# Performance work log

Hardware: AMD Instinct MI355X
Metric: run time of the kernel (lower is better)

Reference implementation:

```python
import jax, jax.numpy as jnp
import numpy as np

B, H, W, D = 4, 64, 64, 256
NH = 8
HD = D // NH        # 32
R = 2               # reduction_ratio
SCALE = 1.0 / np.sqrt(HD).astype(np.float32)
EPS = 1e-5


def _layernorm(x, g, b):
    m = jnp.mean(x, axis=-1, keepdims=True)
    v = jnp.mean((x - m) ** 2, axis=-1, keepdims=True)
    return (x - m) * jax.lax.rsqrt(v + EPS) * g + b


def setup_inputs() -> dict:
    key = jax.random.key(0)
    ks = jax.random.split(key, 8)
    s = 0.02
    return {
        "x": jax.random.normal(ks[0], (B, H, W, D), jnp.float32),
        "de": jax.random.normal(ks[1], (B, H, W, D), jnp.float32),  # unused by module
        "ln1_g": jnp.ones((D,), jnp.float32),
        "ln1_b": jnp.zeros((D,), jnp.float32),
        "Wq": jax.random.normal(ks[2], (D, D), jnp.float32) * s,
        "bq": jnp.zeros((D,), jnp.float32),
        "Wk": jax.random.normal(ks[3], (D, D), jnp.float32) * s,
        "bk": jnp.zeros((D,), jnp.float32),
        "Wv": jax.random.normal(ks[4], (D, D), jnp.float32) * s,
        "bv": jnp.zeros((D,), jnp.float32),
        "Wmean": jax.random.normal(ks[5], (D, D), jnp.float32) * s,  # no bias
        "ln2_g": jnp.ones((D,), jnp.float32),
        "ln2_b": jnp.zeros((D,), jnp.float32),
        "Wo": jax.random.normal(ks[6], (D, D), jnp.float32) * s,
        "bo": jnp.zeros((D,), jnp.float32),
    }


def reference(x, de, ln1_g, ln1_b, Wq, bq, Wk, bk, Wv, bv, Wmean, ln2_g, ln2_b, Wo, bo):
    b, h, w, d = x.shape
    identity = x
    x_norm = _layernorm(x, ln1_g, ln1_b)
    q = x_norm @ Wq + bq                                   # [b,h,w,d]
    # shift_size == 0 -> no roll. Block-mean pool K/V by factor R.
    x_red = jnp.mean(x.reshape(b, h // R, R, w // R, R, d), axis=(2, 4))  # [b,h/R,w/R,d]
    x_red = x_red @ Wmean
    x_red_norm = _layernorm(x_red, ln2_g, ln2_b)
    k = x_red_norm @ Wk + bk
    v = x_red_norm @ Wv + bv
    # split heads: [b, NH, N, HD]
    qf = q.reshape(b, h * w, NH, HD).transpose(0, 2, 1, 3)
    kf = k.reshape(b, (h // R) * (w // R), NH, HD).transpose(0, 2, 1, 3)
    vf = v.reshape(b, (h // R) * (w // R), NH, HD).transpose(0, 2, 1, 3)
    attn = jax.nn.softmax(jnp.einsum('bhqd,bhkd->bhqk', qf, kf) * SCALE, axis=-1)
    out = jnp.einsum('bhqk,bhkd->bhqd', attn, vf)          # [b,NH,N,HD]
    out = out.transpose(0, 2, 1, 3).reshape(b, h, w, d)
    out = out @ Wo + bo
    out = out + identity
    return out, attn
```

## Files before the change

### kernel.cpp

```cpp
#include <hip/hip_runtime.h>

typedef __bf16 bf16x8 __attribute__((ext_vector_type(8)));
typedef __bf16 bf16x4 __attribute__((ext_vector_type(4)));
typedef float f32x4 __attribute__((ext_vector_type(4)));

#define SCALE 0.17677669529663687f

template<int MODE>
__device__ __forceinline__ void gemm_body(const __bf16* __restrict__ A,
    const __bf16* __restrict__ Wt, const float* __restrict__ bias,
    const float* __restrict__ resid, void* __restrict__ Cout,
    int bx, int by, int tid) {
  const int w = tid >> 6, l = tid & 63;
  const int col = l & 15, quad = l >> 4;
  const int row0 = bx * 64 + w * 16;
  const int col0 = by * 64;
  f32x4 acc[4] = {{0.f,0.f,0.f,0.f},{0.f,0.f,0.f,0.f},{0.f,0.f,0.f,0.f},{0.f,0.f,0.f,0.f}};
  const __bf16* ap = A + (size_t)(row0 + col) * 256 + quad * 8;
  #pragma unroll
  for (int ks = 0; ks < 8; ++ks) {
    bf16x8 af = *(const bf16x8*)(ap + ks * 32);
    #pragma unroll
    for (int n = 0; n < 4; ++n) {
      bf16x8 bf = *(const bf16x8*)(Wt + (size_t)(col0 + n * 16 + col) * 256 + ks * 32 + quad * 8);
      acc[n] = __builtin_amdgcn_mfma_f32_16x16x32_bf16(af, bf, acc[n], 0, 0, 0);
    }
  }
  const int rbase = row0 + quad * 4;
  #pragma unroll
  for (int n = 0; n < 4; ++n) {
    const int cc = col0 + n * 16 + col;
    const float bv = bias ? bias[cc] : 0.0f;
    if (MODE == 0) {
      __bf16* C = (__bf16*)Cout;
      #pragma unroll
      for (int r = 0; r < 4; ++r)
        C[(size_t)(rbase + r) * 256 + cc] = (__bf16)(acc[n][r] + bv);
    } else if (MODE == 1) {
      __bf16* C = (__bf16*)Cout;
      const int bb2 = rbase >> 10, tl = rbase & 1023;
      bf16x4 o4;
      #pragma unroll
      for (int r = 0; r < 4; ++r) o4[r] = (__bf16)(acc[n][r] + bv);
      *(bf16x4*)(C + ((size_t)(bb2 * 256 + cc)) * 1024 + tl) = o4;
    } else {
      float* C = (float*)Cout;
      #pragma unroll
      for (int r = 0; r < 4; ++r) {
        size_t off = (size_t)(rbase + r) * 256 + cc;
        C[off] = acc[n][r] + bv + resid[off];
      }
    }
  }
}

__global__ __launch_bounds__(256) void prep_kernel(
    const float* __restrict__ W0, const float* __restrict__ W1,
    const float* __restrict__ W2, const float* __restrict__ W3,
    const float* __restrict__ W4,
    __bf16* __restrict__ T0, __bf16* __restrict__ T1,
    __bf16* __restrict__ T2, __bf16* __restrict__ T3,
    __bf16* __restrict__ T4,
    const float* __restrict__ x, const float* __restrict__ g1,
    const float* __restrict__ b1, __bf16* __restrict__ xn,
    __bf16* __restrict__ xp) {
  const int blk = blockIdx.x, tid = threadIdx.x;
  if (blk < 1280) {
    int which = blk >> 8;
    const float* W = which == 0 ? W0 : which == 1 ? W1 : which == 2 ? W2 : which == 3 ? W3 : W4;
    __bf16* T = which == 0 ? T0 : which == 1 ? T1 : which == 2 ? T2 : which == 3 ? T3 : T4;
    int id = (blk & 255) * 256 + tid;
    int kk = id >> 8, n = id & 255;
    T[n * 256 + kk] = (__bf16)W[id];
  } else if (blk < 5376) {
    int wid = ((blk - 1280) * 256 + tid) >> 6;
    int lane = tid & 63;
    const float4 v = *(const float4*)(x + (size_t)wid * 256 + lane * 4);
    float s = v.x + v.y + v.z + v.w;
    #pragma unroll
    for (int off = 32; off; off >>= 1) s += __shfl_down(s, off);
    float mean = __shfl(s, 0) * (1.0f / 256.0f);
    float dx = v.x - mean, dy = v.y - mean, dz = v.z - mean, dw = v.w - mean;
    float vs = dx * dx + dy * dy + dz * dz + dw * dw;
    #pragma unroll
    for (int off = 32; off; off >>= 1) vs += __shfl_down(vs, off);
    float rstd = rsqrtf(__shfl(vs, 0) * (1.0f / 256.0f) + 1e-5f);
    const float4 gg = *(const float4*)(g1 + lane * 4);
    const float4 bv = *(const float4*)(b1 + lane * 4);
    bf16x4 o4;
    o4[0] = (__bf16)(dx * rstd * gg.x + bv.x);
    o4[1] = (__bf16)(dy * rstd * gg.y + bv.y);
    o4[2] = (__bf16)(dz * rstd * gg.z + bv.z);
    o4[3] = (__bf16)(dw * rstd * gg.w + bv.w);
    *(bf16x4*)(xn + (size_t)wid * 256 + lane * 4) = o4;
  } else {
    int idx = (blk - 5376) * 256 + tid;
    int t = idx >> 6, c4 = (idx & 63) << 2;
    int b = t >> 10, rem = t & 1023;
    int i = rem >> 5, j = rem & 31;
    size_t base = ((size_t)b * 4096 + i * 128 + j * 2) * 256 + c4;
    float4 a0 = *(const float4*)(x + base);
    float4 a1 = *(const float4*)(x + base + 256);
    float4 a2 = *(const float4*)(x + base + 16384);
    float4 a3 = *(const float4*)(x + base + 16640);
    bf16x4 o4;
    o4[0] = (__bf16)(0.25f * (a0.x + a1.x + a2.x + a3.x));
    o4[1] = (__bf16)(0.25f * (a0.y + a1.y + a2.y + a3.y));
    o4[2] = (__bf16)(0.25f * (a0.z + a1.z + a2.z + a3.z));
    o4[3] = (__bf16)(0.25f * (a0.w + a1.w + a2.w + a3.w));
    *(bf16x4*)(xp + (size_t)t * 256 + c4) = o4;
  }
}

__global__ __launch_bounds__(256) void qm_kernel(
    const __bf16* __restrict__ xn, const __bf16* __restrict__ WtQ,
    const float* __restrict__ bq, __bf16* __restrict__ qb,
    const __bf16* __restrict__ xp, const __bf16* __restrict__ WtM,
    const float* __restrict__ g2, const float* __restrict__ b2,
    __bf16* __restrict__ xr) {
  const int blk = blockIdx.x, tid = threadIdx.x;
  if (blk < 1024) {
    gemm_body<0>(xn, WtQ, bq, nullptr, qb, blk & 255, blk >> 8, tid);
    return;
  }
  const int w = tid >> 6, l = tid & 63;
  const int col = l & 15, quad = l >> 4;
  const int row0 = (blk - 1024) * 64 + w * 16;
  f32x4 acc[16];
  #pragma unroll
  for (int n = 0; n < 16; ++n) acc[n] = (f32x4){0.f, 0.f, 0.f, 0.f};
  const __bf16* ap = xp + (size_t)(row0 + col) * 256 + quad * 8;
  #pragma unroll
  for (int ks = 0; ks < 8; ++ks) {
    bf16x8 af = *(const bf16x8*)(ap + ks * 32);
    #pragma unroll
    for (int n = 0; n < 16; ++n) {
      bf16x8 bf = *(const bf16x8*)(WtM + (size_t)(n * 16 + col) * 256 + ks * 32 + quad * 8);
      acc[n] = __builtin_amdgcn_mfma_f32_16x16x32_bf16(af, bf, acc[n], 0, 0, 0);
    }
  }
  #pragma unroll
  for (int r = 0; r < 4; ++r) {
    float s = 0.f;
    #pragma unroll
    for (int n = 0; n < 16; ++n) s += acc[n][r];
    #pragma unroll
    for (int m = 1; m < 16; m <<= 1) s += __shfl_xor(s, m);
    float mean = s * (1.0f / 256.0f);
    float vs = 0.f;
    #pragma unroll
    for (int n = 0; n < 16; ++n) { float d = acc[n][r] - mean; vs += d * d; }
    #pragma unroll
    for (int m = 1; m < 16; m <<= 1) vs += __shfl_xor(vs, m);
    float rstd = rsqrtf(vs * (1.0f / 256.0f) + 1e-5f);
    int row = row0 + quad * 4 + r;
    #pragma unroll
    for (int n = 0; n < 16; ++n) {
      int cc = n * 16 + col;
      xr[(size_t)row * 256 + cc] = (__bf16)((acc[n][r] - mean) * rstd * g2[cc] + b2[cc]);
    }
  }
}

__global__ __launch_bounds__(256) void kv_kernel(
    const __bf16* __restrict__ xr, const __bf16* __restrict__ WtK,
    const float* __restrict__ bk, __bf16* __restrict__ kbuf,
    const __bf16* __restrict__ WtV, const float* __restrict__ bv,
    __bf16* __restrict__ vTb) {
  const int blk = blockIdx.x, tid = threadIdx.x;
  if (blk < 256) gemm_body<0>(xr, WtK, bk, nullptr, kbuf, blk & 63, blk >> 6, tid);
  else { int k = blk - 256; gemm_body<1>(xr, WtV, bv, nullptr, vTb, k & 63, k >> 6, tid); }
}

__global__ __launch_bounds__(256) void o_kernel(
    const __bf16* __restrict__ oat, const __bf16* __restrict__ WtO,
    const float* __restrict__ bo, const float* __restrict__ resid,
    float* __restrict__ out) {
  gemm_body<2>(oat, WtO, bo, resid, out, blockIdx.x, blockIdx.y, threadIdx.x);
}

__device__ __forceinline__ int swz(int row, int c) {
  return row * 1024 + (c ^ ((row & 7) << 2));
}

__global__ __launch_bounds__(256) void attn_fused(
    const __bf16* __restrict__ q, const __bf16* __restrict__ kb,
    const __bf16* __restrict__ vT, float* __restrict__ attn,
    __bf16* __restrict__ oat) {
  __shared__ float Ss[16 * 1024];
  __shared__ float part[64 * 32];
  __shared__ float inv_s[16];
  const int tid = threadIdx.x;
  const int w = tid >> 6, l = tid & 63;
  const int col = l & 15, quad = l >> 4;
  const int bh = blockIdx.y, b = bh >> 3, h = bh & 7;
  const int q0 = blockIdx.x * 16;

  bf16x8 qf = *(const bf16x8*)(q + ((size_t)(b * 4096 + q0 + col)) * 256 + h * 32 + quad * 8);
  const __bf16* kbase = kb + ((size_t)(b * 1024 + col)) * 256 + h * 32 + quad * 8;
  #pragma unroll 4
  for (int t = 0; t < 16; ++t) {
    int j0 = w * 256 + t * 16;
    bf16x8 kf = *(const bf16x8*)(kbase + (size_t)j0 * 256);
    f32x4 c = {0.f, 0.f, 0.f, 0.f};
    c = __builtin_amdgcn_mfma_f32_16x16x32_bf16(qf, kf, c, 0, 0, 0);
    #pragma unroll
    for (int r = 0; r < 4; ++r)
      Ss[swz(quad * 4 + r, j0 + col)] = c[r] * SCALE;
  }
  __syncthreads();

  #pragma unroll
  for (int rr = 0; rr < 4; ++rr) {
    int row = w * 4 + rr;
    float4 v4[4];
    float m = -1e30f;
    #pragma unroll
    for (int i = 0; i < 4; ++i) {
      v4[i] = *(const float4*)(&Ss[swz(row, i * 256 + l * 4)]);
      m = fmaxf(m, fmaxf(fmaxf(v4[i].x, v4[i].y), fmaxf(v4[i].z, v4[i].w)));
    }
    #pragma unroll
    for (int off = 32; off; off >>= 1) m = fmaxf(m, __shfl_down(m, off));
    m = __shfl(m, 0);
    float s = 0.f;
    #pragma unroll
    for (int i = 0; i < 4; ++i) {
      v4[i].x = __expf(v4[i].x - m); v4[i].y = __expf(v4[i].y - m);
      v4[i].z = __expf(v4[i].z - m); v4[i].w = __expf(v4[i].w - m);
      s += v4[i].x + v4[i].y + v4[i].z + v4[i].w;
    }
    #pragma unroll
    for (int off = 32; off; off >>= 1) s += __shfl_down(s, off);
    if (l == 0) inv_s[row] = 1.0f / __shfl(s, 0);
    #pragma unroll
    for (int i = 0; i < 4; ++i)
      *(float4*)(&Ss[swz(row, i * 256 + l * 4)]) = v4[i];
  }
  __syncthreads();

  {
    float* abase = attn + ((size_t)bh * 4096 + q0) * 1024;
    int c4 = tid * 4;
    #pragma unroll 4
    for (int row = 0; row < 16; ++row) {
      f32x4 pv = *(const f32x4*)(&Ss[swz(row, c4)]);
      float iv = inv_s[row];
      pv[0] *= iv; pv[1] *= iv; pv[2] *= iv; pv[3] *= iv;
      __builtin_nontemporal_store(pv, (f32x4*)(abase + (size_t)row * 1024 + c4));
    }
  }

  f32x4 a0 = {0.f, 0.f, 0.f, 0.f}, a1 = {0.f, 0.f, 0.f, 0.f};
  const __bf16* v0p = vT + ((size_t)(b * 256 + h * 32 + col)) * 1024;
  const __bf16* v1p = v0p + 16 * 1024;
  #pragma unroll 2
  for (int s8 = 0; s8 < 8; ++s8) {
    int k0 = w * 256 + s8 * 32;
    int c0 = k0 + quad * 8;
    f32x4 p0 = *(const f32x4*)(&Ss[swz(col, c0)]);
    f32x4 p1 = *(const f32x4*)(&Ss[swz(col, c0 + 4)]);
    bf16x8 af;
    af[0] = (__bf16)p0[0]; af[1] = (__bf16)p0[1]; af[2] = (__bf16)p0[2]; af[3] = (__bf16)p0[3];
    af[4] = (__bf16)p1[0]; af[5] = (__bf16)p1[1]; af[6] = (__bf16)p1[2]; af[7] = (__bf16)p1[3];
    bf16x8 b0 = *(const bf16x8*)(v0p + k0 + quad * 8);
    bf16x8 b1 = *(const bf16x8*)(v1p + k0 + quad * 8);
    a0 = __builtin_amdgcn_mfma_f32_16x16x32_bf16(af, b0, a0, 0, 0, 0);
    a1 = __builtin_amdgcn_mfma_f32_16x16x32_bf16(af, b1, a1, 0, 0, 0);
  }

  #pragma unroll
  for (int r = 0; r < 4; ++r) {
    part[(w * 16 + quad * 4 + r) * 32 + col] = a0[r];
    part[(w * 16 + quad * 4 + r) * 32 + 16 + col] = a1[r];
  }
  __syncthreads();
  int idx = tid;
  #pragma unroll
  for (int it = 0; it < 2; ++it, idx += 256) {
    int row = idx >> 5, d = idx & 31;
    float sum = (part[row * 32 + d] + part[(16 + row) * 32 + d]
               + part[(32 + row) * 32 + d] + part[(48 + row) * 32 + d]) * inv_s[row];
    oat[((size_t)(b * 4096 + q0 + row)) * 256 + h * 32 + d] = (__bf16)sum;
  }
}

extern "C" void kernel_launch(void* const* d_in, const int* in_sizes, int n_in,
                              void* d_out, int out_size, void* d_ws, size_t ws_size,
                              hipStream_t stream) {
  (void)in_sizes; (void)n_in; (void)out_size; (void)ws_size;
  const float* x     = (const float*)d_in[0];
  const float* ln1_g = (const float*)d_in[2];
  const float* ln1_b = (const float*)d_in[3];
  const float* Wq    = (const float*)d_in[4];
  const float* bq    = (const float*)d_in[5];
  const float* Wk    = (const float*)d_in[6];
  const float* bk    = (const float*)d_in[7];
  const float* Wv    = (const float*)d_in[8];
  const float* bv    = (const float*)d_in[9];
  const float* Wmean = (const float*)d_in[10];
  const float* ln2_g = (const float*)d_in[11];
  const float* ln2_b = (const float*)d_in[12];
  const float* Wo    = (const float*)d_in[13];
  const float* bo    = (const float*)d_in[14];

  float* out  = (float*)d_out;
  float* attn = out + 4194304;

  __bf16* w0   = (__bf16*)d_ws;
  __bf16* xn   = w0;
  __bf16* qb   = w0 + 4194304;
  __bf16* oat  = w0 + 8388608;
  __bf16* xp   = w0 + 12582912;
  __bf16* xr   = w0 + 14680064;
  __bf16* kbuf = w0 + 15728640;
  __bf16* vTb  = w0 + 16777216;
  __bf16* WtQ  = w0 + 17825792;
  __bf16* WtK  = WtQ + 65536;
  __bf16* WtV  = WtK + 65536;
  __bf16* WtM  = WtV + 65536;
  __bf16* WtO  = WtM + 65536;

  prep_kernel<<<6400, 256, 0, stream>>>(Wq, Wk, Wv, Wmean, Wo,
                                        WtQ, WtK, WtV, WtM, WtO,
                                        x, ln1_g, ln1_b, xn, xp);
  qm_kernel<<<1088, 256, 0, stream>>>(xn, WtQ, bq, qb, xp, WtM, ln2_g, ln2_b, xr);
  kv_kernel<<<512, 256, 0, stream>>>(xr, WtK, bk, kbuf, WtV, bv, vTb);
  attn_fused<<<dim3(256, 32), 256, 0, stream>>>(qb, kbuf, vTb, attn, oat);
  o_kernel<<<dim3(256, 4), 256, 0, stream>>>(oat, WtO, bo, x, out);
}
```

Measured before the change: 744.9 us.

## Fuse softmax normalization with attn store, two query tiles per block, coalesce output epilogue

The attention kernel now normalizes probabilities in registers inside the softmax pass and writes them to the global attn tensor straight from there. This removes the separate shared-memory read-back pass and the inv_s array, and the PV result no longer needs rescaling. Each block now handles two 16-row query tiles in sequence, which halves the grid and reuses the per-block K/V pointer setup. The output projection stages its accumulators through shared memory so the residual load and the fp32 output store use coalesced float4 accesses. The trade-offs are less block-level parallelism and extra LDS traffic in the output kernel.

```diff
diff --git a/kernel.cpp b/kernel.cpp
--- a/kernel.cpp
+++ b/kernel.cpp
@@ -9,8 +9,7 @@
 template<int MODE>
 __device__ __forceinline__ void gemm_body(const __bf16* __restrict__ A,
     const __bf16* __restrict__ Wt, const float* __restrict__ bias,
-    const float* __restrict__ resid, void* __restrict__ Cout,
-    int bx, int by, int tid) {
+    void* __restrict__ Cout, int bx, int by, int tid) {
   const int w = tid >> 6, l = tid & 63;
   const int col = l & 15, quad = l >> 4;
   const int row0 = bx * 64 + w * 16;
@@ -36,20 +35,13 @@
       #pragma unroll
       for (int r = 0; r < 4; ++r)
         C[(size_t)(rbase + r) * 256 + cc] = (__bf16)(acc[n][r] + bv);
-    } else if (MODE == 1) {
+    } else {
       __bf16* C = (__bf16*)Cout;
       const int bb2 = rbase >> 10, tl = rbase & 1023;
       bf16x4 o4;
       #pragma unroll
       for (int r = 0; r < 4; ++r) o4[r] = (__bf16)(acc[n][r] + bv);
       *(bf16x4*)(C + ((size_t)(bb2 * 256 + cc)) * 1024 + tl) = o4;
-    } else {
-      float* C = (float*)Cout;
-      #pragma unroll
-      for (int r = 0; r < 4; ++r) {
-        size_t off = (size_t)(rbase + r) * 256 + cc;
-        C[off] = acc[n][r] + bv + resid[off];
-      }
     }
   }
 }
@@ -120,7 +112,7 @@
     __bf16* __restrict__ xr) {
   const int blk = blockIdx.x, tid = threadIdx.x;
   if (blk < 1024) {
-    gemm_body<0>(xn, WtQ, bq, nullptr, qb, blk & 255, blk >> 8, tid);
+    gemm_body<0>(xn, WtQ, bq, qb, blk & 255, blk >> 8, tid);
     return;
   }
   const int w = tid >> 6, l = tid & 63;
@@ -168,15 +160,50 @@
     const __bf16* __restrict__ WtV, const float* __restrict__ bv,
     __bf16* __restrict__ vTb) {
   const int blk = blockIdx.x, tid = threadIdx.x;
-  if (blk < 256) gemm_body<0>(xr, WtK, bk, nullptr, kbuf, blk & 63, blk >> 6, tid);
-  else { int k = blk - 256; gemm_body<1>(xr, WtV, bv, nullptr, vTb, k & 63, k >> 6, tid); }
+  if (blk < 256) gemm_body<0>(xr, WtK, bk, kbuf, blk & 63, blk >> 6, tid);
+  else { int k = blk - 256; gemm_body<1>(xr, WtV, bv, vTb, k & 63, k >> 6, tid); }
 }
 
 __global__ __launch_bounds__(256) void o_kernel(
     const __bf16* __restrict__ oat, const __bf16* __restrict__ WtO,
     const float* __restrict__ bo, const float* __restrict__ resid,
     float* __restrict__ out) {
-  gemm_body<2>(oat, WtO, bo, resid, out, blockIdx.x, blockIdx.y, threadIdx.x);
+  __shared__ float sm[4][16][68];
+  const int tid = threadIdx.x;
+  const int w = tid >> 6, l = tid & 63;
+  const int col = l & 15, quad = l >> 4;
+  const int row0 = blockIdx.x * 64 + w * 16;
+  const int col0 = blockIdx.y * 64;
+  f32x4 acc[4] = {{0.f,0.f,0.f,0.f},{0.f,0.f,0.f,0.f},{0.f,0.f,0.f,0.f},{0.f,0.f,0.f,0.f}};
+  const __bf16* ap = oat + (size_t)(row0 + col) * 256 + quad * 8;
+  #pragma unroll
+  for (int ks = 0; ks < 8; ++ks) {
+    bf16x8 af = *(const bf16x8*)(ap + ks * 32);
+    #pragma unroll
+    for (int n = 0; n < 4; ++n) {
+      bf16x8 bf = *(const bf16x8*)(WtO + (size_t)(col0 + n * 16 + col) * 256 + ks * 32 + quad * 8);
+      acc[n] = __builtin_amdgcn_mfma_f32_16x16x32_bf16(af, bf, acc[n], 0, 0, 0);
+    }
+  }
+  #pragma unroll
+  for (int n = 0; n < 4; ++n) {
+    const float bv = bo[col0 + n * 16 + col];
+    #pragma unroll
+    for (int r = 0; r < 4; ++r)
+      sm[w][quad * 4 + r][n * 16 + col] = acc[n][r] + bv;
+  }
+  #pragma unroll
+  for (int i = 0; i < 4; ++i) {
+    int lr = i * 4 + quad;
+    int f4 = l & 15;
+    size_t off = (size_t)(row0 + lr) * 256 + col0 + f4 * 4;
+    float4 rv = *(const float4*)(resid + off);
+    const float* sp = &sm[w][lr][f4 * 4];
+    float4 ov;
+    ov.x = sp[0] + rv.x; ov.y = sp[1] + rv.y;
+    ov.z = sp[2] + rv.z; ov.w = sp[3] + rv.w;
+    *(float4*)(out + off) = ov;
+  }
 }
 
 __device__ __forceinline__ int swz(int row, int c) {
@@ -189,99 +216,94 @@
     __bf16* __restrict__ oat) {
   __shared__ float Ss[16 * 1024];
   __shared__ float part[64 * 32];
-  __shared__ float inv_s[16];
   const int tid = threadIdx.x;
   const int w = tid >> 6, l = tid & 63;
   const int col = l & 15, quad = l >> 4;
   const int bh = blockIdx.y, b = bh >> 3, h = bh & 7;
-  const int q0 = blockIdx.x * 16;
-
-  bf16x8 qf = *(const bf16x8*)(q + ((size_t)(b * 4096 + q0 + col)) * 256 + h * 32 + quad * 8);
   const __bf16* kbase = kb + ((size_t)(b * 1024 + col)) * 256 + h * 32 + quad * 8;
-  #pragma unroll 4
-  for (int t = 0; t < 16; ++t) {
-    int j0 = w * 256 + t * 16;
-    bf16x8 kf = *(const bf16x8*)(kbase + (size_t)j0 * 256);
-    f32x4 c = {0.f, 0.f, 0.f, 0.f};
-    c = __builtin_amdgcn_mfma_f32_16x16x32_bf16(qf, kf, c, 0, 0, 0);
-    #pragma unroll
-    for (int r = 0; r < 4; ++r)
-      Ss[swz(quad * 4 + r, j0 + col)] = c[r] * SCALE;
-  }
-  __syncthreads();
-
-  #pragma unroll
-  for (int rr = 0; rr < 4; ++rr) {
-    int row = w * 4 + rr;
-    float4 v4[4];
-    float m = -1e30f;
-    #pragma unroll
-    for (int i = 0; i < 4; ++i) {
-      v4[i] = *(const float4*)(&Ss[swz(row, i * 256 + l * 4)]);
-      m = fmaxf(m, fmaxf(fmaxf(v4[i].x, v4[i].y), fmaxf(v4[i].z, v4[i].w)));
-    }
-    #pragma unroll
-    for (int off = 32; off; off >>= 1) m = fmaxf(m, __shfl_down(m, off));
-    m = __shfl(m, 0);
-    float s = 0.f;
-    #pragma unroll
-    for (int i = 0; i < 4; ++i) {
-      v4[i].x = __expf(v4[i].x - m); v4[i].y = __expf(v4[i].y - m);
-      v4[i].z = __expf(v4[i].z - m); v4[i].w = __expf(v4[i].w - m);
-      s += v4[i].x + v4[i].y + v4[i].z + v4[i].w;
-    }
-    #pragma unroll
-    for (int off = 32; off; off >>= 1) s += __shfl_down(s, off);
-    if (l == 0) inv_s[row] = 1.0f / __shfl(s, 0);
-    #pragma unroll
-    for (int i = 0; i < 4; ++i)
-      *(float4*)(&Ss[swz(row, i * 256 + l * 4)]) = v4[i];
-  }
-  __syncthreads();
-
-  {
-    float* abase = attn + ((size_t)bh * 4096 + q0) * 1024;
-    int c4 = tid * 4;
-    #pragma unroll 4
-    for (int row = 0; row < 16; ++row) {
-      f32x4 pv = *(const f32x4*)(&Ss[swz(row, c4)]);
-      float iv = inv_s[row];
-      pv[0] *= iv; pv[1] *= iv; pv[2] *= iv; pv[3] *= iv;
-      __builtin_nontemporal_store(pv, (f32x4*)(abase + (size_t)row * 1024 + c4));
-    }
-  }
-
-  f32x4 a0 = {0.f, 0.f, 0.f, 0.f}, a1 = {0.f, 0.f, 0.f, 0.f};
   const __bf16* v0p = vT + ((size_t)(b * 256 + h * 32 + col)) * 1024;
   const __bf16* v1p = v0p + 16 * 1024;
-  #pragma unroll 2
-  for (int s8 = 0; s8 < 8; ++s8) {
-    int k0 = w * 256 + s8 * 32;
-    int c0 = k0 + quad * 8;
-    f32x4 p0 = *(const f32x4*)(&Ss[swz(col, c0)]);
-    f32x4 p1 = *(const f32x4*)(&Ss[swz(col, c0 + 4)]);
-    bf16x8 af;
-    af[0] = (__bf16)p0[0]; af[1] = (__bf16)p0[1]; af[2] = (__bf16)p0[2]; af[3] = (__bf16)p0[3];
-    af[4] = (__bf16)p1[0]; af[5] = (__bf16)p1[1]; af[6] = (__bf16)p1[2]; af[7] = (__bf16)p1[3];
-    bf16x8 b0 = *(const bf16x8*)(v0p + k0 + quad * 8);
-    bf16x8 b1 = *(const bf16x8*)(v1p + k0 + quad * 8);
-    a0 = __builtin_amdgcn_mfma_f32_16x16x32_bf16(af, b0, a0, 0, 0, 0);
-    a1 = __builtin_amdgcn_mfma_f32_16x16x32_bf16(af, b1, a1, 0, 0, 0);
-  }
-
-  #pragma unroll
-  for (int r = 0; r < 4; ++r) {
-    part[(w * 16 + quad * 4 + r) * 32 + col] = a0[r];
-    part[(w * 16 + quad * 4 + r) * 32 + 16 + col] = a1[r];
-  }
-  __syncthreads();
-  int idx = tid;
-  #pragma unroll
-  for (int it = 0; it < 2; ++it, idx += 256) {
-    int row = idx >> 5, d = idx & 31;
-    float sum = (part[row * 32 + d] + part[(16 + row) * 32 + d]
-               + part[(32 + row) * 32 + d] + part[(48 + row) * 32 + d]) * inv_s[row];
-    oat[((size_t)(b * 4096 + q0 + row)) * 256 + h * 32 + d] = (__bf16)sum;
+
+  for (int tile = 0; tile < 2; ++tile) {
+    const int q0 = blockIdx.x * 32 + tile * 16;
+
+    bf16x8 qf = *(const bf16x8*)(q + ((size_t)(b * 4096 + q0 + col)) * 256 + h * 32 + quad * 8);
+    #pragma unroll 4
+    for (int t = 0; t < 16; ++t) {
+      int j0 = w * 256 + t * 16;
+      bf16x8 kf = *(const bf16x8*)(kbase + (size_t)j0 * 256);
+      f32x4 c = {0.f, 0.f, 0.f, 0.f};
+      c = __builtin_amdgcn_mfma_f32_16x16x32_bf16(qf, kf, c, 0, 0, 0);
+      #pragma unroll
+      for (int r = 0; r < 4; ++r)
+        Ss[swz(quad * 4 + r, j0 + col)] = c[r] * SCALE;
+    }
+    __syncthreads();
+
+    float* abase = attn + ((size_t)bh * 4096 + q0) * 1024;
+    #pragma unroll
+    for (int rr = 0; rr < 4; ++rr) {
+      int row = w * 4 + rr;
+      f32x4 v4[4];
+      float m = -1e30f;
+      #pragma unroll
+      for (int i = 0; i < 4; ++i) {
+        v4[i] = *(const f32x4*)(&Ss[swz(row, i * 256 + l * 4)]);
+        m = fmaxf(m, fmaxf(fmaxf(v4[i][0], v4[i][1]), fmaxf(v4[i][2], v4[i][3])));
+      }
+      #pragma unroll
+      for (int off = 32; off; off >>= 1) m = fmaxf(m, __shfl_down(m, off));
+      m = __shfl(m, 0);
+      float s = 0.f;
+      #pragma unroll
+      for (int i = 0; i < 4; ++i) {
+        v4[i][0] = __expf(v4[i][0] - m); v4[i][1] = __expf(v4[i][1] - m);
+        v4[i][2] = __expf(v4[i][2] - m); v4[i][3] = __expf(v4[i][3] - m);
+        s += v4[i][0] + v4[i][1] + v4[i][2] + v4[i][3];
+      }
+      #pragma unroll
+      for (int off = 32; off; off >>= 1) s += __shfl_down(s, off);
+      float inv = 1.0f / __shfl(s, 0);
+      float* arow = abase + (size_t)row * 1024;
+      #pragma unroll
+      for (int i = 0; i < 4; ++i) {
+        v4[i][0] *= inv; v4[i][1] *= inv; v4[i][2] *= inv; v4[i][3] *= inv;
+        *(f32x4*)(&Ss[swz(row, i * 256 + l * 4)]) = v4[i];
+        __builtin_nontemporal_store(v4[i], (f32x4*)(arow + i * 256 + l * 4));
+      }
+    }
+    __syncthreads();
+
+    f32x4 a0 = {0.f, 0.f, 0.f, 0.f}, a1 = {0.f, 0.f, 0.f, 0.f};
+    #pragma unroll 2
+    for (int s8 = 0; s8 < 8; ++s8) {
+      int k0 = w * 256 + s8 * 32;
+      int c0 = k0 + quad * 8;
+      f32x4 p0 = *(const f32x4*)(&Ss[swz(col, c0)]);
+      f32x4 p1 = *(const f32x4*)(&Ss[swz(col, c0 + 4)]);
+      bf16x8 af;
+      af[0] = (__bf16)p0[0]; af[1] = (__bf16)p0[1]; af[2] = (__bf16)p0[2]; af[3] = (__bf16)p0[3];
+      af[4] = (__bf16)p1[0]; af[5] = (__bf16)p1[1]; af[6] = (__bf16)p1[2]; af[7] = (__bf16)p1[3];
+      bf16x8 b0 = *(const bf16x8*)(v0p + k0 + quad * 8);
+      bf16x8 b1 = *(const bf16x8*)(v1p + k0 + quad * 8);
+      a0 = __builtin_amdgcn_mfma_f32_16x16x32_bf16(af, b0, a0, 0, 0, 0);
+      a1 = __builtin_amdgcn_mfma_f32_16x16x32_bf16(af, b1, a1, 0, 0, 0);
+    }
+
+    #pragma unroll
+    for (int r = 0; r < 4; ++r) {
+      part[(w * 16 + quad * 4 + r) * 32 + col] = a0[r];
+      part[(w * 16 + quad * 4 + r) * 32 + 16 + col] = a1[r];
+    }
+    __syncthreads();
+    int idx = tid;
+    #pragma unroll
+    for (int it = 0; it < 2; ++it, idx += 256) {
+      int row = idx >> 5, d = idx & 31;
+      float sum = part[row * 32 + d] + part[(16 + row) * 32 + d]
+                + part[(32 + row) * 32 + d] + part[(48 + row) * 32 + d];
+      oat[((size_t)(b * 4096 + q0 + row)) * 256 + h * 32 + d] = (__bf16)sum;
+    }
   }
 }
 
@@ -326,6 +348,6 @@
                                         x, ln1_g, ln1_b, xn, xp);
   qm_kernel<<<1088, 256, 0, stream>>>(xn, WtQ, bq, qb, xp, WtM, ln2_g, ln2_b, xr);
   kv_kernel<<<512, 256, 0, stream>>>(xr, WtK, bk, kbuf, WtV, bv, vTb);
-  attn_fused<<<dim3(256, 32), 256, 0, stream>>>(qb, kbuf, vTb, attn, oat);
+  attn_fused<<<dim3(128, 32), 256, 0, stream>>>(qb, kbuf, vTb, attn, oat);
   o_kernel<<<dim3(256, 4), 256, 0, stream>>>(oat, WtO, bo, x, out);
 }
```

Measured after the change: 716.1 us. -3.9%, faster.
